# Kernel tuning notes

Hardware: AMD Instinct MI355X
Metric: run time of the kernel (lower is better)

## Reference

```python
import jax, jax.numpy as jnp
import numpy as np

B, S, C = 2, 2048, 1024
U, H = 1024, 16
FFH = int(U * 4.0)
NEG = -1e9
EPS = 1e-5


def setup_inputs() -> dict:
    key = jax.random.key(0)
    ks = jax.random.split(key, 16)
    w = lambda k, sh: jax.random.normal(k, sh, dtype=jnp.float32) * 0.02
    return {
        'x': jax.random.normal(ks[0], (B, S, C), dtype=jnp.float32),
        'wq': w(ks[1], (C, U)), 'bq': jnp.zeros((U,), jnp.float32),
        'wk': w(ks[2], (C, U)), 'bk': jnp.zeros((U,), jnp.float32),
        'wv': w(ks[3], (C, U)), 'bv': jnp.zeros((U,), jnp.float32),
        'wf1': w(ks[4], (U, FFH)), 'bf1': jnp.zeros((FFH,), jnp.float32),
        'wf2': w(ks[5], (FFH, U)), 'bf2': jnp.zeros((U,), jnp.float32),
        'ln_g': jnp.ones((S, U), jnp.float32), 'ln_b': jnp.zeros((S, U), jnp.float32),
        'ffln_g': jnp.ones((S, U), jnp.float32), 'ffln_b': jnp.zeros((S, U), jnp.float32),
    }


def _ln2d(x, g, b):
    # LayerNorm over last two dims ([len_ts, units]) as in nn.LayerNorm([S, U])
    m = jnp.mean(x, axis=(-2, -1), keepdims=True)
    v = jnp.mean(jnp.square(x - m), axis=(-2, -1), keepdims=True)
    return (x - m) * jax.lax.rsqrt(v + EPS) * g + b


def reference(x, wq, bq, wk, bk, wv, bv, wf1, bf1, wf2, bf2, ln_g, ln_b, ffln_g, ffln_b):
    dh = U // H
    Q = (x @ wq + bq).reshape(B, S, H, dh)
    K = (x @ wk + bk).reshape(B, S, H, dh)
    V = (x @ wv + bv).reshape(B, S, H, dh)
    scores = jnp.einsum('bqhd,bkhd->bhqk', Q, K) / jnp.sqrt(jnp.float32(dh))
    mask = jnp.tril(jnp.ones((S, S), dtype=bool))  # causal tril buffer
    scores = jnp.where(mask, scores, NEG)
    attn = jax.nn.softmax(scores, axis=-1)
    out = jnp.einsum('bhqk,bkhd->bqhd', attn, V).reshape(B, S, U)
    out = out + x  # residual
    out = _ln2d(out, ln_g, ln_b)
    ff = jax.nn.relu(out @ wf1 + bf1) @ wf2 + bf2
    out = _ln2d(out + ff, ffln_g, ffln_b)
    return out
```

## Files before the change

### kernel.cpp

```cpp
#include <hip/hip_runtime.h>
#include <hip/hip_bf16.h>

typedef short s16x8 __attribute__((ext_vector_type(8)));
typedef float f32x4 __attribute__((ext_vector_type(4)));
typedef float f32x16 __attribute__((ext_vector_type(16)));
typedef unsigned short u16x4 __attribute__((ext_vector_type(4)));
typedef unsigned u32x4 __attribute__((ext_vector_type(4)));

#define DEV static __device__ __forceinline__

DEV unsigned short f2bf(float f) {
  __hip_bfloat16 h = __float2bfloat16(f);
  return *reinterpret_cast<unsigned short*>(&h);
}
DEV float bf2f(unsigned short u) {
  union { unsigned u; float f; } v; v.u = (unsigned)u << 16; return v.f;
}

#define GLDS16(src, dst) \
  __builtin_amdgcn_global_load_lds((const __attribute__((address_space(1))) void*)(src), \
                                   (__attribute__((address_space(3))) void*)(dst), 16, 0, 0)

#define MFMA(a, b, c) __builtin_amdgcn_mfma_f32_16x16x32_bf16((a), (b), (c), 0, 0, 0)
#define MFMA32(a, b, c) __builtin_amdgcn_mfma_f32_32x32x16_bf16((a), (b), (c), 0, 0, 0)

__global__ __launch_bounds__(256) void k_f32_to_bf16(const float* __restrict__ in,
                                                     unsigned short* __restrict__ out, int n4) {
  int i = blockIdx.x * 256 + threadIdx.x;
  if (i >= n4) return;
  float4 v = ((const float4*)in)[i];
  u16x4 o; o.x = f2bf(v.x); o.y = f2bf(v.y); o.z = f2bf(v.z); o.w = f2bf(v.w);
  ((u16x4*)out)[i] = o;
}

__global__ __launch_bounds__(256) void k_transpose_w(const float* __restrict__ W,
                                                     unsigned short* __restrict__ Wt,
                                                     int K, int N, float scale) {
  __shared__ float t[64][65];
  int k0 = blockIdx.x * 64, n0 = blockIdx.y * 64;
  int tid = threadIdx.x;
#pragma unroll
  for (int i = 0; i < 16; ++i) {
    int idx = tid + i * 256; int r = idx >> 6, c = idx & 63;
    t[r][c] = W[(size_t)(k0 + r) * N + (n0 + c)];
  }
  __syncthreads();
#pragma unroll
  for (int i = 0; i < 16; ++i) {
    int idx = tid + i * 256; int r = idx >> 6, c = idx & 63;
    Wt[(size_t)(n0 + r) * K + (k0 + c)] = f2bf(t[c][r] * scale);
  }
}

__global__ __launch_bounds__(256) void k_transpose_w3(
    const float* __restrict__ W0, const float* __restrict__ W1,
    const float* __restrict__ W2, unsigned short* __restrict__ Wt, float s0) {
  __shared__ float t[64][65];
  int z = blockIdx.z;
  const float* W = (z == 0) ? W0 : (z == 1) ? W1 : W2;
  float scale = (z == 0) ? s0 : 1.0f;
  unsigned short* dst = Wt + (size_t)z * 1024 * 1024;
  int k0 = blockIdx.x * 64, n0 = blockIdx.y * 64;
  int tid = threadIdx.x;
#pragma unroll
  for (int i = 0; i < 16; ++i) {
    int idx = tid + i * 256; int r = idx >> 6, c = idx & 63;
    t[r][c] = W[(size_t)(k0 + r) * 1024 + (n0 + c)];
  }
  __syncthreads();
#pragma unroll
  for (int i = 0; i < 16; ++i) {
    int idx = tid + i * 256; int r = idx >> 6, c = idx & 63;
    dst[(size_t)(n0 + r) * 1024 + (k0 + c)] = f2bf(t[c][r] * scale);
  }
}

__global__ void k_concat3(const float* __restrict__ a, const float* __restrict__ b,
                          const float* __restrict__ c, float* __restrict__ out, int n, float sa) {
  int i = blockIdx.x * 256 + threadIdx.x;
  if (i >= 3 * n) return;
  int j = (i < n) ? i : (i < 2 * n ? i - n : i - 2 * n);
  out[i] = (i < n) ? a[j] * sa : (i < 2 * n ? b[j] : c[j]);
}

template <int MODE>
__global__ __launch_bounds__(512, 2) void k_gemm8(
    const unsigned short* __restrict__ A, int lda,
    const unsigned short* __restrict__ Bt, int ldb,
    const float* __restrict__ bias,
    unsigned short* __restrict__ Cb, float* __restrict__ Cf, int ldc,
    int K, int nnt, size_t zstride,
    unsigned short* __restrict__ Cq, unsigned short* __restrict__ Ck,
    unsigned short* __restrict__ Cv) {
  __shared__ __align__(16) unsigned short As[2 * 2 * 8192];
  __shared__ __align__(16) unsigned short Bs[2 * 2 * 8192];
  int nwg = gridDim.x;
  int bid = blockIdx.x;
  int cpx = nwg >> 3;
  int swz = (bid & 7) * cpx + (bid >> 3);
  int mt = swz / nnt, nt = swz % nnt;
  int m0 = mt * 256, n0 = nt * 256;
  int tid = threadIdx.x, w = tid >> 6, l = tid & 63;
  int wm = (w >> 2) * 128, wn = (w & 3) * 64;
  int kb = blockIdx.z * K;

  int sr = tid >> 2;
  int gsrc = (tid & 3) ^ ((sr >> 1) & 3);
  const unsigned short* Ag0 = A + (size_t)(m0 + sr) * lda + kb + gsrc * 8;
  const unsigned short* Ag1 = Ag0 + (size_t)128 * lda;
  const unsigned short* Bg0 = Bt + (size_t)(n0 + sr) * ldb + kb + gsrc * 8;
  const unsigned short* Bg1 = Bg0 + (size_t)128 * ldb;

#define STG_A(t, kh) do { int _c = (t) * 64 + (kh) * 32; int _d = ((((t) & 1) * 2 + (kh)) * 8192); \
    GLDS16(Ag0 + _c, &As[_d + tid * 8]); GLDS16(Ag1 + _c, &As[_d + 4096 + tid * 8]); } while (0)
#define STG_B(t, kh) do { int _c = (t) * 64 + (kh) * 32; int _d = ((((t) & 1) * 2 + (kh)) * 8192); \
    GLDS16(Bg0 + _c, &Bs[_d + tid * 8]); GLDS16(Bg1 + _c, &Bs[_d + 4096 + tid * 8]); } while (0)

  int lswz = (l >> 1) & 3;
  int acol = ((l >> 4) ^ lswz) * 8;
  const unsigned short* Afr = &As[(wm + (l & 15)) * 32 + acol];
  const unsigned short* Bfr = &Bs[(wn + (l & 15)) * 32 + acol];

  f32x4 acc[8][4] = {};
  int nkt = K >> 6;

  STG_A(0, 0); STG_B(0, 0); STG_A(0, 1); STG_B(0, 1); STG_A(1, 0); STG_B(1, 0);
  asm volatile("s_waitcnt vmcnt(4)" ::: "memory");
  __builtin_amdgcn_s_barrier();
  __builtin_amdgcn_sched_barrier(0);

  for (int t = 0; t < nkt; ++t) {
    int cur = t & 1, rem = nkt - t;
    const unsigned short* ab = Afr + cur * 16384;
    const unsigned short* bb = Bfr + cur * 16384;
    s16x8 af[4], bf[4], afn[4], bfn[4];
    if (t + 1 < nkt) STG_A(t + 1, 1);
#pragma unroll
    for (int nr = 0; nr < 4; ++nr) bf[nr] = *(const s16x8*)(bb + nr * 512);
#pragma unroll
    for (int mr = 0; mr < 4; ++mr) af[mr] = *(const s16x8*)(ab + mr * 512);
    __builtin_amdgcn_s_setprio(1);
#pragma unroll
    for (int mr = 0; mr < 4; ++mr)
#pragma unroll
      for (int nr = 0; nr < 4; ++nr)
        acc[mr][nr] = MFMA(af[mr], bf[nr], acc[mr][nr]);
    __builtin_amdgcn_s_setprio(0);
    if (t + 1 < nkt) STG_B(t + 1, 1);
#pragma unroll
    for (int mr = 0; mr < 4; ++mr) af[mr] = *(const s16x8*)(ab + 2048 + mr * 512);
    __builtin_amdgcn_s_setprio(1);
#pragma unroll
    for (int mr = 0; mr < 4; ++mr)
#pragma unroll
      for (int nr = 0; nr < 4; ++nr)
        acc[mr + 4][nr] = MFMA(af[mr], bf[nr], acc[mr + 4][nr]);
    __builtin_amdgcn_s_setprio(0);
#pragma unroll
    for (int nr = 0; nr < 4; ++nr) bfn[nr] = *(const s16x8*)(bb + 8192 + nr * 512);
#pragma unroll
    for (int mr = 0; mr < 4; ++mr) afn[mr] = *(const s16x8*)(ab + 8192 + mr * 512);
#pragma unroll
    for (int mr = 0; mr < 4; ++mr) af[mr] = *(const s16x8*)(ab + 8192 + 2048 + mr * 512);
    if (rem >= 2) { asm volatile("s_waitcnt vmcnt(4)" ::: "memory"); }
    else          { asm volatile("s_waitcnt vmcnt(0)" ::: "memory"); }
    __builtin_amdgcn_s_barrier();
    if (t + 2 < nkt) STG_A(t + 2, 0);
    __builtin_amdgcn_s_setprio(1);
#pragma unroll
    for (int mr = 0; mr < 4; ++mr)
#pragma unroll
      for (int nr = 0; nr < 4; ++nr)
        acc[mr][nr] = MFMA(afn[mr], bfn[nr], acc[mr][nr]);
    __builtin_amdgcn_s_setprio(0);
    if (t + 2 < nkt) STG_B(t + 2, 0);
    __builtin_amdgcn_s_setprio(1);
#pragma unroll
    for (int mr = 0; mr < 4; ++mr)
#pragma unroll
      for (int nr = 0; nr < 4; ++nr)
        acc[mr + 4][nr] = MFMA(af[mr], bfn[nr], acc[mr + 4][nr]);
    __builtin_amdgcn_s_setprio(0);
    if (rem >= 3) { asm volatile("s_waitcnt vmcnt(4)" ::: "memory"); }
    else          { asm volatile("s_waitcnt vmcnt(0)" ::: "memory"); }
    __builtin_amdgcn_s_barrier();
    __builtin_amdgcn_sched_barrier(0);
  }
#undef STG_A
#undef STG_B

  if (MODE == 4) {
    if (nt < 8) {
      unsigned short* dst = (nt < 4) ? Cq : Ck;
      int cb = (nt < 4) ? 0 : 1024;
#pragma unroll
      for (int mr = 0; mr < 8; ++mr) {
        int rb = m0 + wm + mr * 16 + (l >> 4) * 4;
#pragma unroll
        for (int nr = 0; nr < 4; ++nr) {
          int col = n0 + wn + nr * 16 + (l & 15);
          float bv = bias[col];
#pragma unroll
          for (int j = 0; j < 4; ++j)
            dst[(size_t)(rb + j) * 1024 + (col - cb)] = f2bf(acc[mr][nr][j] + bv);
        }
      }
    } else {
#pragma unroll
      for (int mr = 0; mr < 8; ++mr) {
        int rb = m0 + wm + mr * 16 + (l >> 4) * 4;
        int b2 = rb >> 11, s2 = rb & 2047;
        int s2p = (s2 & ~12) | ((s2 & 4) << 1) | ((s2 & 8) >> 1);
#pragma unroll
        for (int nr = 0; nr < 4; ++nr) {
          int col2 = n0 - 2048 + wn + nr * 16 + (l & 15);
          float bv = bias[col2 + 2048];
          u16x4 pk;
#pragma unroll
          for (int j = 0; j < 4; ++j) ((unsigned short*)&pk)[j] = f2bf(acc[mr][nr][j] + bv);
          *(u16x4*)(Cv + ((size_t)((b2 * 16 + (col2 >> 6)) * 64 + (col2 & 63))) * 2048 + s2p) = pk;
        }
      }
    }
    return;
  }
  unsigned short* Cbz = (MODE == 3) ? (Cb + zstride * blockIdx.z) : Cb;
#pragma unroll
  for (int mr = 0; mr < 8; ++mr) {
    int rb = m0 + wm + mr * 16 + (l >> 4) * 4;
#pragma unroll
    for (int nr = 0; nr < 4; ++nr) {
      int col = n0 + wn + nr * 16 + (l & 15);
      float bv = (MODE == 3) ? 0.f : bias[col];
#pragma unroll
      for (int j = 0; j < 4; ++j) {
        float v = acc[mr][nr][j] + bv;
        size_t off = (size_t)(rb + j) * ldc + col;
        if (MODE == 1) v = fmaxf(v, 0.f);
        Cbz[off] = f2bf(v);
      }
    }
  }
}

__global__ __launch_bounds__(256) void k_ff2_reduce(
    unsigned short* __restrict__ slices, const float* __restrict__ bias,
    const unsigned short* __restrict__ resid, float* __restrict__ partials) {
  __shared__ float red[8];
  int i = blockIdx.x;
  size_t rb = (size_t)i * 4096;
  int c = threadIdx.x * 4;
  u16x4 a0 = *(const u16x4*)(slices + rb + c);
  u16x4 a1 = *(const u16x4*)(slices + rb + 1024 + c);
  u16x4 a2 = *(const u16x4*)(slices + rb + 2048 + c);
  u16x4 a3 = *(const u16x4*)(slices + rb + 3072 + c);
  float4 bv = *(const float4*)(bias + c);
  u16x4 rv = *(const u16x4*)(resid + (size_t)i * 1024 + c);
  float4 o;
  o.x = bf2f(a0.x) + bf2f(a1.x) + bf2f(a2.x) + bf2f(a3.x) + bv.x + bf2f(rv.x);
  o.y = bf2f(a0.y) + bf2f(a1.y) + bf2f(a2.y) + bf2f(a3.y) + bv.y + bf2f(rv.y);
  o.z = bf2f(a0.z) + bf2f(a1.z) + bf2f(a2.z) + bf2f(a3.z) + bv.z + bf2f(rv.z);
  o.w = bf2f(a0.w) + bf2f(a1.w) + bf2f(a2.w) + bf2f(a3.w) + bv.w + bf2f(rv.w);
  __syncthreads();
  *(float4*)((float*)slices + (size_t)i * 2048 + c) = o;
  float bsum = o.x + o.y + o.z + o.w;
  float bsq = o.x * o.x + o.y * o.y + o.z * o.z + o.w * o.w;
  int wv = threadIdx.x >> 6, lv = threadIdx.x & 63;
#pragma unroll
  for (int mk = 1; mk < 64; mk <<= 1) { bsum += __shfl_xor(bsum, mk); bsq += __shfl_xor(bsq, mk); }
  if (lv == 0) { red[wv] = bsum; red[4 + wv] = bsq; }
  __syncthreads();
  if (threadIdx.x == 0) {
    partials[i * 2] = red[0] + red[1] + red[2] + red[3];
    partials[i * 2 + 1] = red[4] + red[5] + red[6] + red[7];
  }
}

__global__ __launch_bounds__(128, 2) void k_attn(
    const unsigned short* __restrict__ Qg, const unsigned short* __restrict__ Kg,
    const unsigned short* __restrict__ Vt,
    const float* __restrict__ x, unsigned short* __restrict__ hpre,
    float* __restrict__ partials, int S, int H) {
  __shared__ __align__(16) unsigned short Ks[2][4096];
  __shared__ __align__(16) unsigned short Vs[2][4096];
  __shared__ float ascr[2][32];
  __shared__ float red[4];
  int bh = blockIdx.x, b = bh >> 4, h = bh & 15;
  const int nqt = S / 64;
  int qt = nqt - 1 - (int)blockIdx.y;
  int tid = threadIdx.x, w = tid >> 6, l = tid & 63;
  int lo = l & 31, hi5 = l >> 5;
  const int U = H * 64;
  const unsigned short* Qb = Qg + (size_t)(b * S) * 1024 + h * 64;
  const unsigned short* Kb = Kg + (size_t)(b * S) * 1024 + h * 64;
  const unsigned short* Vb = Vt + (size_t)bh * 64 * S;

  int sg_r[4], sg_c[4];
#pragma unroll
  for (int it = 0; it < 4; ++it) {
    int g = it * 128 + tid;
    sg_r[it] = g >> 3;
    sg_c[it] = ((g & 7) ^ ((g >> 3) & 7)) * 8;
  }
#define STG_K(kt) do { int _kn = (kt) * 64, _bf = (kt) & 1; \
    _Pragma("unroll") for (int it = 0; it < 4; ++it) \
      GLDS16(Kb + (size_t)(_kn + sg_r[it]) * 1024 + sg_c[it], &Ks[_bf][(it * 128 + tid) * 8]); } while (0)
#define STG_V(kt) do { int _kn = (kt) * 64, _bf = (kt) & 1; \
    _Pragma("unroll") for (int it = 0; it < 4; ++it) \
      GLDS16(Vb + (size_t)sg_r[it] * S + _kn + sg_c[it], &Vs[_bf][(it * 128 + tid) * 8]); } while (0)

  int qrow = qt * 64 + w * 32 + lo;
  s16x8 qf[4];
#pragma unroll
  for (int s = 0; s < 4; ++s)
    qf[s] = *(const s16x8*)(Qb + (size_t)qrow * 1024 + s * 16 + hi5 * 8);

  int krow[16];
#pragma unroll
  for (int r = 0; r < 16; ++r) krow[r] = (r & 3) + 8 * (r >> 2) + 4 * hi5;

  f32x16 o0 = {}, o1 = {};
  float m = -1e30f, lsum = 0.f;
  f32x16 scA0, scA1, scB0, scB1;

#define QK_T(S0, S1, T) do { \
    S0 = (f32x16)(0.0f); S1 = (f32x16)(0.0f); \
    const unsigned short* _kp = &Ks[(T) & 1][0]; \
    __builtin_amdgcn_s_setprio(1); \
    _Pragma("unroll") for (int s = 0; s < 4; ++s) { \
      int gc = ((2 * s + hi5) ^ (lo & 7)) * 8; \
      s16x8 kf0 = *(const s16x8*)&_kp[lo * 64 + gc]; \
      s16x8 kf1 = *(const s16x8*)&_kp[(32 + lo) * 64 + gc]; \
      S0 = MFMA32(kf0, qf[s], S0); \
      S1 = MFMA32(kf1, qf[s], S1); } \
    __builtin_amdgcn_s_setprio(0); } while (0)

#define SMPV(S0, S1, T, DOMASK) do { \
    if (DOMASK) { int wq = w * 32 + lo; \
      _Pragma("unroll") for (int r = 0; r < 16; ++r) { \
        if (krow[r] > wq) S0[r] = -1e30f; \
        if (krow[r] + 32 > wq) S1[r] = -1e30f; } } \
    float mx = S0[0]; \
    _Pragma("unroll") for (int r = 1; r < 16; ++r) mx = fmaxf(mx, S0[r]); \
    _Pragma("unroll") for (int r = 0; r < 16; ++r) mx = fmaxf(mx, S1[r]); \
    mx = fmaxf(mx, __shfl_xor(mx, 32)); \
    if (__ballot(mx > m + 11.5415603f)) { \
      float mnew = fmaxf(m, mx); \
      float alpha = __builtin_amdgcn_exp2f(m - mnew); \
      m = mnew; lsum *= alpha; \
      if (l < 32) ascr[w][lo] = alpha; \
      _Pragma("unroll") for (int r = 0; r < 16; ++r) { \
        float aj = ascr[w][krow[r]]; o0[r] *= aj; o1[r] *= aj; } } \
    float rs = 0.f; unsigned wk0[8], wk1[8]; \
    _Pragma("unroll") for (int j = 0; j < 8; ++j) { \
      float p0 = __builtin_amdgcn_exp2f(S0[2 * j] - m); \
      float p1 = __builtin_amdgcn_exp2f(S0[2 * j + 1] - m); \
      rs += p0 + p1; wk0[j] = (unsigned)f2bf(p0) | ((unsigned)f2bf(p1) << 16); \
      float p2 = __builtin_amdgcn_exp2f(S1[2 * j] - m); \
      float p3 = __builtin_amdgcn_exp2f(S1[2 * j + 1] - m); \
      rs += p2 + p3; wk1[j] = (unsigned)f2bf(p2) | ((unsigned)f2bf(p3) << 16); } \
    rs += __shfl_xor(rs, 32); lsum += rs; \
    __builtin_amdgcn_s_setprio(1); \
    _Pragma("unroll") for (int s = 0; s < 4; ++s) { \
      u32x4 paw; \
      if (s == 0)      { paw.x = wk0[0]; paw.y = wk0[1]; paw.z = wk0[2]; paw.w = wk0[3]; } \
      else if (s == 1) { paw.x = wk0[4]; paw.y = wk0[5]; paw.z = wk0[6]; paw.w = wk0[7]; } \
      else if (s == 2) { paw.x = wk1[0]; paw.y = wk1[1]; paw.z = wk1[2]; paw.w = wk1[3]; } \
      else             { paw.x = wk1[4]; paw.y = wk1[5]; paw.z = wk1[6]; paw.w = wk1[7]; } \
      s16x8 pa = *(s16x8*)&paw; \
      int gc = ((2 * s + hi5) ^ (lo & 7)) * 8; \
      s16x8 vf0 = *(const s16x8*)&Vs[(T) & 1][lo * 64 + gc]; \
      s16x8 vf1 = *(const s16x8*)&Vs[(T) & 1][(32 + lo) * 64 + gc]; \
      o0 = MFMA32(pa, vf0, o0); \
      o1 = MFMA32(pa, vf1, o1); } \
    __builtin_amdgcn_s_setprio(0); \
  } while (0)

#define BODY(O0, O1, I0, I1, T) do { \
    asm volatile("s_waitcnt vmcnt(4)" ::: "memory"); \
    __builtin_amdgcn_s_barrier(); \
    __builtin_amdgcn_sched_barrier(0); \
    if ((T) + 1 <= qt) STG_K((T) + 1); \
    QK_T(O0, O1, (T)); \
    SMPV(I0, I1, (T) - 1, false); \
    asm volatile("s_waitcnt lgkmcnt(0)" ::: "memory"); \
    __builtin_amdgcn_sched_barrier(0); \
    __builtin_amdgcn_s_barrier(); \
    __builtin_amdgcn_sched_barrier(0); \
    if ((T) + 1 <= qt) STG_V((T) + 1); \
  } while (0)

  STG_K(0); STG_V(0);
  if (qt >= 1) {
    STG_K(1); STG_V(1);
    asm volatile("s_waitcnt vmcnt(8)" ::: "memory");
  } else {
    asm volatile("s_waitcnt vmcnt(4)" ::: "memory");
  }
  __builtin_amdgcn_s_barrier();
  __builtin_amdgcn_sched_barrier(0);
  QK_T(scA0, scA1, 0);
  asm volatile("s_waitcnt lgkmcnt(0)" ::: "memory");
  __builtin_amdgcn_sched_barrier(0);

  int t = 1;
  for (; t + 1 <= qt; t += 2) {
    BODY(scB0, scB1, scA0, scA1, t);
    BODY(scA0, scA1, scB0, scB1, t + 1);
  }
  if (t <= qt) {
    BODY(scB0, scB1, scA0, scA1, t);
    asm volatile("s_waitcnt vmcnt(0)" ::: "memory");
    __builtin_amdgcn_sched_barrier(0);
    SMPV(scB0, scB1, qt, true);
  } else {
    asm volatile("s_waitcnt vmcnt(0)" ::: "memory");
    __builtin_amdgcn_sched_barrier(0);
    SMPV(scA0, scA1, qt, true);
  }

  if (l < 32) ascr[w][lo] = 1.f / lsum;
  float bsum = 0.f, bsq = 0.f;
  unsigned short* hb = hpre + (size_t)(b * S) * U + h * 64;
  const float* xb = x + (size_t)(b * S) * U + h * 64;
#pragma unroll
  for (int r = 0; r < 16; ++r) {
    float inv = ascr[w][krow[r]];
    int srow = qt * 64 + w * 32 + krow[r];
    size_t base = (size_t)srow * U + lo;
    float v0 = o0[r] * inv + xb[base];
    float v1 = o1[r] * inv + xb[base + 32];
    hb[base] = f2bf(v0);
    hb[base + 32] = f2bf(v1);
    bsum += v0 + v1; bsq += v0 * v0 + v1 * v1;
  }
#pragma unroll
  for (int mk = 1; mk < 64; mk <<= 1) { bsum += __shfl_xor(bsum, mk); bsq += __shfl_xor(bsq, mk); }
  if (l == 0) { red[w * 2] = bsum; red[w * 2 + 1] = bsq; }
  __syncthreads();
  if (tid == 0) {
    int pi = b * (H * nqt) + h * nqt + qt;
    partials[pi * 2] = red[0] + red[2];
    partials[pi * 2 + 1] = red[1] + red[3];
  }
#undef STG_K
#undef STG_V
#undef QK_T
#undef SMPV
#undef BODY
}

__global__ __launch_bounds__(256) void k_ln_stats(const float* __restrict__ partials, int nper,
                                                  float* __restrict__ stats, float invN) {
  int b = blockIdx.x, tid = threadIdx.x;
  float s = 0.f, q = 0.f;
  for (int i = tid; i < nper; i += 256) { s += partials[(b * nper + i) * 2]; q += partials[(b * nper + i) * 2 + 1]; }
#pragma unroll
  for (int mk = 1; mk < 64; mk <<= 1) { s += __shfl_xor(s, mk); q += __shfl_xor(q, mk); }
  __shared__ float red[8];
  int w = tid >> 6, l = tid & 63;
  if (l == 0) { red[w] = s; red[4 + w] = q; }
  __syncthreads();
  if (tid == 0) {
    s = red[0] + red[1] + red[2] + red[3];
    q = red[4] + red[5] + red[6] + red[7];
    float m = s * invN, var = q * invN - m * m;
    stats[b * 2] = m; stats[b * 2 + 1] = rsqrtf(var + 1e-5f);
  }
}

__global__ __launch_bounds__(256) void k_ln_apply_b(
    const unsigned short* __restrict__ src, const float* __restrict__ stats,
    const float* __restrict__ g, const float* __restrict__ bt,
    unsigned short* __restrict__ outb, int SU) {
  int b = blockIdx.y;
  int idx = (blockIdx.x * 256 + threadIdx.x) * 4;
  float m = stats[b * 2], r = stats[b * 2 + 1];
  u16x4 v4 = *(const u16x4*)(src + (size_t)b * SU + idx);
  float4 gg = *(const float4*)(g + idx);
  float4 bb = *(const float4*)(bt + idx);
  u16x4 ob;
  ob.x = f2bf((bf2f(v4.x) - m) * r * gg.x + bb.x);
  ob.y = f2bf((bf2f(v4.y) - m) * r * gg.y + bb.y);
  ob.z = f2bf((bf2f(v4.z) - m) * r * gg.z + bb.z);
  ob.w = f2bf((bf2f(v4.w) - m) * r * gg.w + bb.w);
  *(u16x4*)(outb + (size_t)b * SU + idx) = ob;
}

__global__ __launch_bounds__(256) void k_ln_apply2(
    const float* __restrict__ src, const float* __restrict__ stats,
    const float* __restrict__ g, const float* __restrict__ bt,
    float* __restrict__ outf) {
  int b = blockIdx.y;
  int row = blockIdx.x;
  int grow = b * 2048 + row;
  int c = threadIdx.x * 4;
  float m = stats[b * 2], r = stats[b * 2 + 1];
  float4 v = *(const float4*)(src + (size_t)grow * 2048 + c);
  float4 gg = *(const float4*)(g + (size_t)row * 1024 + c);
  float4 bb = *(const float4*)(bt + (size_t)row * 1024 + c);
  float4 o;
  o.x = (v.x - m) * r * gg.x + bb.x;
  o.y = (v.y - m) * r * gg.y + bb.y;
  o.z = (v.z - m) * r * gg.z + bb.z;
  o.w = (v.w - m) * r * gg.w + bb.w;
  *(float4*)(outf + (size_t)grow * 1024 + c) = o;
}

extern "C" void kernel_launch(void* const* d_in, const int* in_sizes, int n_in,
                              void* d_out, int out_size, void* d_ws, size_t ws_size,
                              hipStream_t stream) {
  (void)in_sizes; (void)n_in; (void)out_size; (void)ws_size;
  const int S = 2048, H = 16;
  const float* x   = (const float*)d_in[0];
  const float* wq  = (const float*)d_in[1];
  const float* bq  = (const float*)d_in[2];
  const float* wk  = (const float*)d_in[3];
  const float* bk  = (const float*)d_in[4];
  const float* wv  = (const float*)d_in[5];
  const float* bv  = (const float*)d_in[6];
  const float* wf1 = (const float*)d_in[7];
  const float* bf1 = (const float*)d_in[8];
  const float* wf2 = (const float*)d_in[9];
  const float* bf2 = (const float*)d_in[10];
  const float* lng = (const float*)d_in[11];
  const float* lnb = (const float*)d_in[12];
  const float* ffg = (const float*)d_in[13];
  const float* ffb = (const float*)d_in[14];

  char* ws = (char*)d_ws;
  unsigned short* wqkvT = (unsigned short*)(ws);
  unsigned short* wf1T  = (unsigned short*)(ws + 6291456);
  unsigned short* wf2T  = (unsigned short*)(ws + 14680064);
  unsigned short* xb    = (unsigned short*)(ws + 23068672);
  unsigned short* qb    = (unsigned short*)(ws + 31457280);
  unsigned short* kbuf  = (unsigned short*)(ws + 39845888);
  unsigned short* vt    = (unsigned short*)(ws + 56623104);
  unsigned short* h1b   = (unsigned short*)(ws + 65011712);
  unsigned short* hpreb = (unsigned short*)(ws + 73400320);
  unsigned short* ff2s  = (unsigned short*)(ws + 73400320);
  unsigned short* f1b   = (unsigned short*)(ws + 23068672);
  float* biasqkv        = (float*)(ws + 106954752);
  float* part_attn      = (float*)(ws + 106967040);
  float* stats1         = (float*)(ws + 106977280);
  float* ffpart2        = (float*)(ws);
  float* stats2         = (float*)(ws + 65536);

  const float qscale = 0.125f * 1.44269504f;
  k_f32_to_bf16<<<4096, 256, 0, stream>>>(x, xb, 4096 * 1024 / 4);
  k_transpose_w3<<<dim3(16, 16, 3), 256, 0, stream>>>(wq, wk, wv, wqkvT, qscale);
  k_transpose_w<<<dim3(16, 64), 256, 0, stream>>>(wf1, wf1T, 1024, 4096, 1.0f);
  k_transpose_w<<<dim3(64, 16), 256, 0, stream>>>(wf2, wf2T, 4096, 1024, 1.0f);
  k_concat3<<<12, 256, 0, stream>>>(bq, bk, bv, biasqkv, 1024, qscale);

  k_gemm8<4><<<dim3(192, 1, 1), 512, 0, stream>>>(xb, 1024, wqkvT, 1024, biasqkv,
      nullptr, nullptr, 0, 1024, 12, 0, qb, kbuf, vt);

  k_attn<<<dim3(32, 32), 128, 0, stream>>>(qb, kbuf, vt, x, hpreb, part_attn, S, H);

  k_ln_stats<<<2, 256, 0, stream>>>(part_attn, 512, stats1, 1.f / (2048.f * 1024.f));
  k_ln_apply_b<<<dim3(2048, 2), 256, 0, stream>>>(hpreb, stats1, lng, lnb, h1b, S * 1024);

  k_gemm8<1><<<dim3(256, 1, 1), 512, 0, stream>>>(h1b, 1024, wf1T, 1024, bf1,
      f1b, nullptr, 4096, 1024, 16, 0, nullptr, nullptr, nullptr);

  k_gemm8<3><<<dim3(64, 1, 4), 512, 0, stream>>>(f1b, 4096, wf2T, 4096, nullptr,
      ff2s, nullptr, 4096, 1024, 4, 1024, nullptr, nullptr, nullptr);

  k_ff2_reduce<<<4096, 256, 0, stream>>>(ff2s, bf2, h1b, ffpart2);

  k_ln_stats<<<2, 256, 0, stream>>>(ffpart2, 2048, stats2, 1.f / (2048.f * 1024.f));
  k_ln_apply2<<<dim3(2048, 2), 256, 0, stream>>>((float*)ff2s, stats2, ffg, ffb, (float*)d_out);
}
```

Before: 217.2 us.

## Use 128-row query tiles with four waves in causal attention kernel

```diff
diff --git a/kernel.cpp b/kernel.cpp
--- a/kernel.cpp
+++ b/kernel.cpp
@@ -276,40 +276,41 @@
   }
 }
 
-__global__ __launch_bounds__(128, 2) void k_attn(
+__global__ __launch_bounds__(256, 2) void k_attn(
     const unsigned short* __restrict__ Qg, const unsigned short* __restrict__ Kg,
     const unsigned short* __restrict__ Vt,
     const float* __restrict__ x, unsigned short* __restrict__ hpre,
     float* __restrict__ partials, int S, int H) {
   __shared__ __align__(16) unsigned short Ks[2][4096];
   __shared__ __align__(16) unsigned short Vs[2][4096];
-  __shared__ float ascr[2][32];
-  __shared__ float red[4];
+  __shared__ float ascr[4][32];
+  __shared__ float red[8];
   int bh = blockIdx.x, b = bh >> 4, h = bh & 15;
-  const int nqt = S / 64;
-  int qt = nqt - 1 - (int)blockIdx.y;
+  int y = (int)blockIdx.y;
+  int qt = (y < 8) ? (15 - y) : (y - 8);
   int tid = threadIdx.x, w = tid >> 6, l = tid & 63;
   int lo = l & 31, hi5 = l >> 5;
   const int U = H * 64;
   const unsigned short* Qb = Qg + (size_t)(b * S) * 1024 + h * 64;
   const unsigned short* Kb = Kg + (size_t)(b * S) * 1024 + h * 64;
   const unsigned short* Vb = Vt + (size_t)bh * 64 * S;
-
-  int sg_r[4], sg_c[4];
-#pragma unroll
-  for (int it = 0; it < 4; ++it) {
-    int g = it * 128 + tid;
+  int tl = 2 * qt + 1;
+
+  int sg_r[2], sg_c[2];
+#pragma unroll
+  for (int it = 0; it < 2; ++it) {
+    int g = it * 256 + tid;
     sg_r[it] = g >> 3;
     sg_c[it] = ((g & 7) ^ ((g >> 3) & 7)) * 8;
   }
 #define STG_K(kt) do { int _kn = (kt) * 64, _bf = (kt) & 1; \
-    _Pragma("unroll") for (int it = 0; it < 4; ++it) \
-      GLDS16(Kb + (size_t)(_kn + sg_r[it]) * 1024 + sg_c[it], &Ks[_bf][(it * 128 + tid) * 8]); } while (0)
+    _Pragma("unroll") for (int it = 0; it < 2; ++it) \
+      GLDS16(Kb + (size_t)(_kn + sg_r[it]) * 1024 + sg_c[it], &Ks[_bf][(it * 256 + tid) * 8]); } while (0)
 #define STG_V(kt) do { int _kn = (kt) * 64, _bf = (kt) & 1; \
-    _Pragma("unroll") for (int it = 0; it < 4; ++it) \
-      GLDS16(Vb + (size_t)sg_r[it] * S + _kn + sg_c[it], &Vs[_bf][(it * 128 + tid) * 8]); } while (0)
-
-  int qrow = qt * 64 + w * 32 + lo;
+    _Pragma("unroll") for (int it = 0; it < 2; ++it) \
+      GLDS16(Vb + (size_t)sg_r[it] * S + _kn + sg_c[it], &Vs[_bf][(it * 256 + tid) * 8]); } while (0)
+
+  int qrow = qt * 128 + w * 32 + lo;
   s16x8 qf[4];
 #pragma unroll
   for (int s = 0; s < 4; ++s)
@@ -318,10 +319,13 @@
   int krow[16];
 #pragma unroll
   for (int r = 0; r < 16; ++r) krow[r] = (r & 3) + 8 * (r >> 2) + 4 * hi5;
+  int wq = w * 32 + lo;
 
   f32x16 o0 = {}, o1 = {};
   float m = -1e30f, lsum = 0.f;
   f32x16 scA0, scA1, scB0, scB1;
+
+#define MBASE(T) (((T) >= 2 * qt) ? ((T) * 64 - qt * 128) : -1)
 
 #define QK_T(S0, S1, T) do { \
     S0 = (f32x16)(0.0f); S1 = (f32x16)(0.0f); \
@@ -335,11 +339,11 @@
       S1 = MFMA32(kf1, qf[s], S1); } \
     __builtin_amdgcn_s_setprio(0); } while (0)
 
-#define SMPV(S0, S1, T, DOMASK) do { \
-    if (DOMASK) { int wq = w * 32 + lo; \
+#define SMPV(S0, S1, T, MB) do { \
+    if ((MB) >= 0) { \
       _Pragma("unroll") for (int r = 0; r < 16; ++r) { \
-        if (krow[r] > wq) S0[r] = -1e30f; \
-        if (krow[r] + 32 > wq) S1[r] = -1e30f; } } \
+        if (krow[r] + (MB) > wq) S0[r] = -1e30f; \
+        if (krow[r] + 32 + (MB) > wq) S1[r] = -1e30f; } } \
     float mx = S0[0]; \
     _Pragma("unroll") for (int r = 1; r < 16; ++r) mx = fmaxf(mx, S0[r]); \
     _Pragma("unroll") for (int r = 0; r < 16; ++r) mx = fmaxf(mx, S1[r]); \
@@ -377,26 +381,21 @@
   } while (0)
 
 #define BODY(O0, O1, I0, I1, T) do { \
-    asm volatile("s_waitcnt vmcnt(4)" ::: "memory"); \
+    asm volatile("s_waitcnt vmcnt(2)" ::: "memory"); \
     __builtin_amdgcn_s_barrier(); \
     __builtin_amdgcn_sched_barrier(0); \
-    if ((T) + 1 <= qt) STG_K((T) + 1); \
+    if ((T) + 1 <= tl) STG_K((T) + 1); \
     QK_T(O0, O1, (T)); \
-    SMPV(I0, I1, (T) - 1, false); \
+    SMPV(I0, I1, (T) - 1, MBASE((T) - 1)); \
     asm volatile("s_waitcnt lgkmcnt(0)" ::: "memory"); \
     __builtin_amdgcn_sched_barrier(0); \
     __builtin_amdgcn_s_barrier(); \
     __builtin_amdgcn_sched_barrier(0); \
-    if ((T) + 1 <= qt) STG_V((T) + 1); \
+    if ((T) + 1 <= tl) STG_V((T) + 1); \
   } while (0)
 
-  STG_K(0); STG_V(0);
-  if (qt >= 1) {
-    STG_K(1); STG_V(1);
-    asm volatile("s_waitcnt vmcnt(8)" ::: "memory");
-  } else {
-    asm volatile("s_waitcnt vmcnt(4)" ::: "memory");
-  }
+  STG_K(0); STG_V(0); STG_K(1); STG_V(1);
+  asm volatile("s_waitcnt vmcnt(4)" ::: "memory");
   __builtin_amdgcn_s_barrier();
   __builtin_amdgcn_sched_barrier(0);
   QK_T(scA0, scA1, 0);
@@ -404,19 +403,19 @@
   __builtin_amdgcn_sched_barrier(0);
 
   int t = 1;
-  for (; t + 1 <= qt; t += 2) {
+  for (; t + 1 <= tl; t += 2) {
     BODY(scB0, scB1, scA0, scA1, t);
     BODY(scA0, scA1, scB0, scB1, t + 1);
   }
-  if (t <= qt) {
+  if (t <= tl) {
     BODY(scB0, scB1, scA0, scA1, t);
     asm volatile("s_waitcnt vmcnt(0)" ::: "memory");
     __builtin_amdgcn_sched_barrier(0);
-    SMPV(scB0, scB1, qt, true);
+    SMPV(scB0, scB1, tl, MBASE(tl));
   } else {
     asm volatile("s_waitcnt vmcnt(0)" ::: "memory");
     __builtin_amdgcn_sched_barrier(0);
-    SMPV(scA0, scA1, qt, true);
+    SMPV(scA0, scA1, tl, MBASE(tl));
   }
 
   if (l < 32) ascr[w][lo] = 1.f / lsum;
@@ -426,7 +425,7 @@
 #pragma unroll
   for (int r = 0; r < 16; ++r) {
     float inv = ascr[w][krow[r]];
-    int srow = qt * 64 + w * 32 + krow[r];
+    int srow = qt * 128 + w * 32 + krow[r];
     size_t base = (size_t)srow * U + lo;
     float v0 = o0[r] * inv + xb[base];
     float v1 = o1[r] * inv + xb[base + 32];
@@ -439,15 +438,16 @@
   if (l == 0) { red[w * 2] = bsum; red[w * 2 + 1] = bsq; }
   __syncthreads();
   if (tid == 0) {
-    int pi = b * (H * nqt) + h * nqt + qt;
-    partials[pi * 2] = red[0] + red[2];
-    partials[pi * 2 + 1] = red[1] + red[3];
+    int pi = b * (H * 16) + h * 16 + qt;
+    partials[pi * 2] = red[0] + red[2] + red[4] + red[6];
+    partials[pi * 2 + 1] = red[1] + red[3] + red[5] + red[7];
   }
 #undef STG_K
 #undef STG_V
 #undef QK_T
 #undef SMPV
 #undef BODY
+#undef MBASE
 }
 
 __global__ __launch_bounds__(256) void k_ln_stats(const float* __restrict__ partials, int nper,
@@ -556,9 +556,9 @@
   k_gemm8<4><<<dim3(192, 1, 1), 512, 0, stream>>>(xb, 1024, wqkvT, 1024, biasqkv,
       nullptr, nullptr, 0, 1024, 12, 0, qb, kbuf, vt);
 
-  k_attn<<<dim3(32, 32), 128, 0, stream>>>(qb, kbuf, vt, x, hpreb, part_attn, S, H);
-
-  k_ln_stats<<<2, 256, 0, stream>>>(part_attn, 512, stats1, 1.f / (2048.f * 1024.f));
+  k_attn<<<dim3(32, 16), 256, 0, stream>>>(qb, kbuf, vt, x, hpreb, part_attn, S, H);
+
+  k_ln_stats<<<2, 256, 0, stream>>>(part_attn, 256, stats1, 1.f / (2048.f * 1024.f));
   k_ln_apply_b<<<dim3(2048, 2), 256, 0, stream>>>(hpreb, stats1, lng, lnb, h1b, S * 1024);
 
   k_gemm8<1><<<dim3(256, 1, 1), 512, 0, stream>>>(h1b, 1024, wf1T, 1024, bf1,
```

After: 212.5 us. -2.2%, faster.
